# Kernel tuning notes

Hardware: AMD Instinct MI355X
Metric: run time of the kernel (lower is better)

The kernel has to match this reference:

```python
import jax, jax.numpy as jnp
import numpy as np

D, E, H, K = 1024, 8, 1024, 2          # d_model, num_experts, hidden_size, top_k
NUM_LAYERS, LB_W, Z_W = 16, 0.01, 0.001
B, S = 2, 2048


def setup_inputs() -> dict:
    key = jax.random.key(0)
    ks = jax.random.split(key, 8)
    s = lambda d: 1.0 / np.sqrt(d)
    return {
        "x": jax.random.normal(ks[0], (B, S, D), jnp.float32),
        "w_router": jax.random.normal(ks[1], (D, E), jnp.float32) * s(D),
        "w1": jax.random.normal(ks[2], (E, D, H), jnp.float32) * s(D),
        "w3": jax.random.normal(ks[3], (E, D, H), jnp.float32) * s(D),
        "w2": jax.random.normal(ks[4], (E, H, D), jnp.float32) * s(H),
        "sw1": jax.random.normal(ks[5], (D, H), jnp.float32) * s(D),
        "sw3": jax.random.normal(ks[6], (D, H), jnp.float32) * s(D),
        "sw2": jax.random.normal(ks[7], (H, D), jnp.float32) * s(H),
    }


def reference(x, w_router, w1, w3, w2, sw1, sw3, sw2):
    b, s_len, _ = x.shape
    xt = x.reshape(-1, D)                       # (N, D) flattened tokens
    n_tok = xt.shape[0]

    # ---- router: softmax over experts, then top-k ----
    logits = xt @ w_router                      # (N, E)
    probs = jax.nn.softmax(logits, axis=-1)
    weights, indices = jax.lax.top_k(probs, K)  # (N, K)

    # combine weights scattered back to dense (N, E) form
    onehot = jax.nn.one_hot(indices, E, dtype=x.dtype)    # (N, K, E)
    cw = jnp.einsum("nk,nke->ne", weights, onehot)       # (N, E)
    counts = jnp.sum(onehot, axis=(0, 1))                 # (E,) tokens per expert

    # ---- expert SwiGLU MLPs (dense dispatch, weighted combine) ----
    g = jnp.einsum("nd,edh->neh", xt, w1)                 # (N, E, H)
    u = jnp.einsum("nd,edh->neh", xt, w3)
    h = jax.nn.silu(g) * u
    eout = jnp.einsum("neh,ehd->ned", h, w2)              # (N, E, D)
    out = jnp.einsum("ne,ned->nd", cw, eout)              # (N, D)

    # ---- shared expert, weighted-sum combine with top_k ----
    shared = (jax.nn.silu(xt @ sw1) * (xt @ sw3)) @ sw2   # (N, D)
    out = (out * K + shared) / (K + 1)

    # ---- aux losses (training mode) ----
    logits32 = logits.astype(jnp.float32)
    scale = E * LB_W / (NUM_LAYERS * n_tok * K)
    lb_loss = scale * jnp.dot(counts.astype(jnp.float32),
                              jax.nn.softmax(logits32, axis=-1).sum(axis=0))
    z_loss = jnp.mean(jnp.square(jax.nn.logsumexp(logits32, axis=-1))) * Z_W

    return out.reshape(b, s_len, D), lb_loss, z_loss
```

## Files before the change

### kernel.cpp

```cpp
#include <hip/hip_runtime.h>

#define NTOK 4096
#define NEXP 8
#define MAXTILES 104

typedef __attribute__((ext_vector_type(8))) short short8;
typedef __attribute__((ext_vector_type(4))) float f32x4;
typedef __attribute__((ext_vector_type(4))) unsigned int uint4v;
typedef __attribute__((ext_vector_type(2))) unsigned int uint2v;

__device__ __forceinline__ unsigned short f2bf(float f) {
  union { float f; unsigned u; } v; v.f = f;
  unsigned u = v.u;
  return (unsigned short)((u + 0x7FFFu + ((u >> 16) & 1u)) >> 16);
}

__device__ __forceinline__ void gll16(const void* g, void* l) {
  __builtin_amdgcn_global_load_lds((const __attribute__((address_space(1))) void*)g,
                                   (__attribute__((address_space(3))) void*)l, 16, 0, 0);
}

__global__ __launch_bounds__(256) void cvt_t_all_k(
    const float* __restrict__ w1, const float* __restrict__ w3, const float* __restrict__ w2,
    const float* __restrict__ sw1, const float* __restrict__ sw3, const float* __restrict__ sw2,
    unsigned short* __restrict__ dst ) {
  __shared__ unsigned short tile[64][65];
  int z = blockIdx.z;
  const float* S;
  if (z < 8) S = w1 + (size_t)z * 1048576;
  else if (z < 16) S = w3 + (size_t)(z - 8) * 1048576;
  else if (z < 24) S = w2 + (size_t)(z - 16) * 1048576;
  else S = (z == 24) ? sw1 : (z == 25) ? sw3 : sw2;
  unsigned short* Dp = dst + (size_t)z * 1048576;
  int r0 = blockIdx.y * 64, c0 = blockIdx.x * 64;
  int t = threadIdx.x;
  int r = t >> 2, cb = (t & 3) * 16;
  const float* sp = S + (size_t)(r0 + r) * 1024 + c0 + cb;
  f32x4 v0 = ((const f32x4*)sp)[0], v1 = ((const f32x4*)sp)[1];
  f32x4 v2 = ((const f32x4*)sp)[2], v3 = ((const f32x4*)sp)[3];
#pragma unroll
  for (int j = 0; j < 4; ++j) {
    tile[r][cb + j] = f2bf(v0[j]);
    tile[r][cb + 4 + j] = f2bf(v1[j]);
    tile[r][cb + 8 + j] = f2bf(v2[j]);
    tile[r][cb + 12 + j] = f2bf(v3[j]);
  }
  __syncthreads();
  unsigned short* dp = Dp + (size_t)(c0 + r) * 1024 + r0 + cb;
  uint4v o0, o1;
#pragma unroll
  for (int j = 0; j < 4; ++j) {
    o0[j] = (unsigned)tile[cb + 2 * j][r] | ((unsigned)tile[cb + 2 * j + 1][r] << 16);
    o1[j] = (unsigned)tile[cb + 8 + 2 * j][r] | ((unsigned)tile[cb + 9 + 2 * j][r] << 16);
  }
  ((uint4v*)dp)[0] = o0;
  ((uint4v*)dp)[1] = o1;
}

__global__ __launch_bounds__(256) void router_k(
    const float* __restrict__ x, const float* __restrict__ wr, unsigned short* __restrict__ xb,
    int* __restrict__ rec, float* __restrict__ wts, float* __restrict__ probs,
    float* __restrict__ lsebuf) {
  int t = threadIdx.x, lane = t & 63, wv = t >> 6;
  int tok = blockIdx.x * 4 + wv;
  const f32x4* x4 = (const f32x4*)(x + (size_t)tok * 1024);
  f32x4 xv[4];
#pragma unroll
  for (int j = 0; j < 4; ++j) xv[j] = x4[j * 64 + lane];

  unsigned short* xo = xb + (size_t)tok * 1024;
#pragma unroll
  for (int j = 0; j < 4; ++j) {
    uint2v o;
    o[0] = (unsigned)f2bf(xv[j][0]) | ((unsigned)f2bf(xv[j][1]) << 16);
    o[1] = (unsigned)f2bf(xv[j][2]) | ((unsigned)f2bf(xv[j][3]) << 16);
    *(uint2v*)(xo + j * 256 + lane * 4) = o;
  }

  float acc[NEXP];
#pragma unroll
  for (int e = 0; e < NEXP; ++e) acc[e] = 0.f;
#pragma unroll
  for (int j = 0; j < 4; ++j) {
    int base = j * 256 + lane * 4;
#pragma unroll
    for (int c = 0; c < 4; ++c) {
      float xf = xv[j][c];
      const f32x4* wp = (const f32x4*)(wr + (size_t)(base + c) * NEXP);
      f32x4 w0 = wp[0], w1 = wp[1];
#pragma unroll
      for (int e = 0; e < 4; ++e) { acc[e] += xf * w0[e]; acc[4 + e] += xf * w1[e]; }
    }
  }
#pragma unroll
  for (int off = 32; off > 0; off >>= 1) {
#pragma unroll
    for (int e = 0; e < NEXP; ++e) acc[e] += __shfl_xor(acc[e], off);
  }

  float mx = acc[0];
#pragma unroll
  for (int e = 1; e < NEXP; ++e) mx = fmaxf(mx, acc[e]);
  float s = 0.f;
#pragma unroll
  for (int e = 0; e < NEXP; ++e) s += __expf(acc[e] - mx);
  float inv = 1.f / s;

  if (lane < NEXP) probs[(size_t)tok * NEXP + lane] = __expf(acc[lane] - mx) * inv;
  if (lane == 0) {
    int i0 = 0; float v0 = acc[0];
#pragma unroll
    for (int e = 1; e < NEXP; ++e) if (acc[e] > v0) { v0 = acc[e]; i0 = e; }
    int i1 = -1; float v1 = -3.4e38f;
#pragma unroll
    for (int e = 0; e < NEXP; ++e) if (e != i0 && acc[e] > v1) { v1 = acc[e]; i1 = e; }
    rec[tok] = i0 | (i1 << 8);
    wts[2 * tok] = __expf(v0 - mx) * inv;
    wts[2 * tok + 1] = __expf(v1 - mx) * inv;
    lsebuf[tok] = mx + __logf(s);
  }
}

__global__ __launch_bounds__(256) void build_k(
    const int* __restrict__ rec, const float* __restrict__ wts, const float* __restrict__ probs,
    const float* __restrict__ lsebuf,
    int* __restrict__ tlist, float* __restrict__ wlist,
    int* __restrict__ counts, float* __restrict__ probsum, float* __restrict__ zsum) {
  __shared__ int lcnt[NEXP];
  __shared__ int gbase[NEXP];
  __shared__ float wProb[4][NEXP];
  __shared__ float wZ[4];
  int t = threadIdx.x, lane = t & 63, wv = t >> 6;
  if (t < NEXP) lcnt[t] = 0;
  __syncthreads();

  int tok = blockIdx.x * 256 + t;
  int r = rec[tok];
  int i0 = r & 255, i1 = (r >> 8) & 255;
  float w0 = wts[2 * tok], w1 = wts[2 * tok + 1];
  int p0 = atomicAdd(&lcnt[i0], 1);
  int p1 = atomicAdd(&lcnt[i1], 1);

  f32x4 pr0 = ((const f32x4*)(probs + (size_t)tok * NEXP))[0];
  f32x4 pr1 = ((const f32x4*)(probs + (size_t)tok * NEXP))[1];
  float lv = lsebuf[tok];
  float z = lv * lv;
#pragma unroll
  for (int off = 32; off > 0; off >>= 1) {
#pragma unroll
    for (int c = 0; c < 4; ++c) {
      pr0[c] += __shfl_xor(pr0[c], off);
      pr1[c] += __shfl_xor(pr1[c], off);
    }
    z += __shfl_xor(z, off);
  }
  if (lane == 0) {
#pragma unroll
    for (int c = 0; c < 4; ++c) { wProb[wv][c] = pr0[c]; wProb[wv][4 + c] = pr1[c]; }
    wZ[wv] = z;
  }
  __syncthreads();

  if (t < NEXP) {
    gbase[t] = atomicAdd(&counts[t], lcnt[t]);
    atomicAdd(&probsum[t], wProb[0][t] + wProb[1][t] + wProb[2][t] + wProb[3][t]);
  }
  if (t == 0) atomicAdd(zsum, wZ[0] + wZ[1] + wZ[2] + wZ[3]);
  __syncthreads();

  int q0 = gbase[i0] + p0, q1 = gbase[i1] + p1;
  tlist[i0 * NTOK + q0] = tok;
  wlist[i0 * NTOK + q0] = w0;
  tlist[i1 * NTOK + q1] = tok | (1 << 16);
  wlist[i1 * NTOK + q1] = w1;
}

__global__ void scan_k(const int* __restrict__ counts, int* __restrict__ ebase, int* __restrict__ tiles) {
  if (threadIdx.x == 0 && blockIdx.x == 0) {
    int a = 0, t = 0;
    for (int e = 0; e < NEXP; ++e) {
      ebase[e] = a;
      int nt = (counts[e] + 127) >> 7;
      for (int i = 0; i < nt; ++i) tiles[t++] = (e << 16) | i;
      a += nt * 128;
    }
    ebase[NEXP] = a;
    for (int i = 0; i < 32; ++i) tiles[t++] = (NEXP << 16) | i;
    ebase[NEXP + 1] = a + NTOK;
    while (t < MAXTILES) tiles[t++] = -1;
  }
}

__global__ __launch_bounds__(256, 2) void gemm1_k(
    const unsigned short* __restrict__ xb,
    const unsigned short* __restrict__ w1T, const unsigned short* __restrict__ w3T,
    const unsigned short* __restrict__ sw1T, const unsigned short* __restrict__ sw3T,
    unsigned short* __restrict__ hout,
    const int* __restrict__ tlist, const int* __restrict__ counts,
    const int* __restrict__ ebase, const int* __restrict__ tiles) {
  int td = tiles[blockIdx.y];
  if (td < 0) return;
  const int e = td >> 16;
  const int m0 = (td & 0xFFFF) << 7;
  const int n0 = blockIdx.x * 64;
  const bool sh = (e == NEXP);
  const int n_e = sh ? NTOK : counts[e];
  const int hb = ebase[e];
  const unsigned short* B1p = sh ? sw1T : w1T + (size_t)e * 1048576;
  const unsigned short* B3p = sh ? sw3T : w3T + (size_t)e * 1048576;
  const int* listp = tlist + e * NTOK;

  __shared__ unsigned short As[4096], Bs1[2048], Bs3[2048];
  const int tid = threadIdx.x, lane = tid & 63, wv = tid >> 6;
  const int wrw = wv >> 1, wc = wv & 1, l16 = lane & 15, lq = lane >> 4;

  const unsigned short* ga0;
  const unsigned short* ga1;
  const unsigned short* gb;
  const unsigned short* gc;
  {
    int c = tid, r = c >> 2, ks = (c & 3) ^ ((r >> 1) & 3);
    int ar = m0 + r;
    int rowA = sh ? ar : (ar < n_e ? (listp[ar] & 0xFFFF) : 0);
    ga0 = xb + (size_t)rowA * 1024 + ks * 8;
  }
  {
    int c = tid + 256, r = c >> 2, ks = (c & 3) ^ ((r >> 1) & 3);
    int ar = m0 + r;
    int rowA = sh ? ar : (ar < n_e ? (listp[ar] & 0xFFFF) : 0);
    ga1 = xb + (size_t)rowA * 1024 + ks * 8;
  }
  {
    int c = tid, r = c >> 2, ks = (c & 3) ^ ((r >> 1) & 3);
    gb = B1p + (size_t)(n0 + r) * 1024 + ks * 8;
    gc = B3p + (size_t)(n0 + r) * 1024 + ks * 8;
  }
  unsigned short* lA0 = As + wv * 512;
  unsigned short* lA1 = As + 2048 + wv * 512;
  unsigned short* lB = Bs1 + wv * 512;
  unsigned short* lC = Bs3 + wv * 512;

  f32x4 accg[4][2], accu[4][2];
#pragma unroll
  for (int mi = 0; mi < 4; ++mi)
#pragma unroll
    for (int ni = 0; ni < 2; ++ni)
#pragma unroll
      for (int r = 0; r < 4; ++r) { accg[mi][ni][r] = 0.f; accu[mi][ni][r] = 0.f; }

  for (int k0 = 0; k0 < 1024; k0 += 32) {
    gll16(ga0, lA0); gll16(ga1, lA1); gll16(gb, lB); gll16(gc, lC);
    ga0 += 32; ga1 += 32; gb += 32; gc += 32;
    __syncthreads();
    short8 af[4], b1f[2], b3f[2];
#pragma unroll
    for (int mi = 0; mi < 4; ++mi) {
      int R = wrw * 64 + mi * 16 + l16;
      int s = lq ^ ((R >> 1) & 3);
      af[mi] = *(const short8*)&As[R * 32 + s * 8];
    }
#pragma unroll
    for (int ni = 0; ni < 2; ++ni) {
      int R = wc * 32 + ni * 16 + l16;
      int s = lq ^ ((R >> 1) & 3);
      b1f[ni] = *(const short8*)&Bs1[R * 32 + s * 8];
      b3f[ni] = *(const short8*)&Bs3[R * 32 + s * 8];
    }
#pragma unroll
    for (int mi = 0; mi < 4; ++mi)
#pragma unroll
      for (int ni = 0; ni < 2; ++ni) {
        accg[mi][ni] = __builtin_amdgcn_mfma_f32_16x16x32_bf16(af[mi], b1f[ni], accg[mi][ni], 0, 0, 0);
        accu[mi][ni] = __builtin_amdgcn_mfma_f32_16x16x32_bf16(af[mi], b3f[ni], accu[mi][ni], 0, 0, 0);
      }
    __syncthreads();
  }

#pragma unroll
  for (int mi = 0; mi < 4; ++mi)
#pragma unroll
    for (int ni = 0; ni < 2; ++ni) {
      int col = n0 + wc * 32 + ni * 16 + l16;
#pragma unroll
      for (int r = 0; r < 4; ++r) {
        int row = m0 + wrw * 64 + mi * 16 + lq * 4 + r;
        float g = accg[mi][ni][r], u = accu[mi][ni][r];
        float h = g / (1.f + __expf(-g)) * u;
        hout[(size_t)(hb + row) * 1024 + col] = (row < n_e) ? f2bf(h) : (unsigned short)0;
      }
    }
}

__global__ __launch_bounds__(256, 2) void gemm2_k(
    const unsigned short* __restrict__ hbuf,
    const unsigned short* __restrict__ w2T, const unsigned short* __restrict__ sw2T,
    float* __restrict__ yout,
    const int* __restrict__ tlist, const float* __restrict__ wlist,
    const int* __restrict__ counts, const int* __restrict__ ebase, const int* __restrict__ tiles) {
  int td = tiles[blockIdx.y];
  if (td < 0) return;
  const int e = td >> 16;
  const int m0 = (td & 0xFFFF) << 7;
  const int n0 = blockIdx.x * 128;
  const bool sh = (e == NEXP);
  const int n_e = sh ? NTOK : counts[e];
  const int hb = ebase[e];
  const unsigned short* Bp = sh ? sw2T : w2T + (size_t)e * 1048576;
  const int* listp = tlist + e * NTOK;

  __shared__ unsigned short As[4096], Bs[4096];
  const int tid = threadIdx.x, lane = tid & 63, wv = tid >> 6;
  const int wrw = wv >> 1, wc = wv & 1, l16 = lane & 15, lq = lane >> 4;

  const unsigned short* ga[2];
  const unsigned short* gb[2];
#pragma unroll
  for (int i = 0; i < 2; ++i) {
    int c = tid + i * 256;
    int r = c >> 2, kc = c & 3;
    int ks = kc ^ ((r >> 1) & 3);
    ga[i] = hbuf + (size_t)(hb + m0 + r) * 1024 + ks * 8;
    gb[i] = Bp + (size_t)(n0 + r) * 1024 + ks * 8;
  }
  unsigned short* lA[2] = {As + wv * 512, As + 2048 + wv * 512};
  unsigned short* lB[2] = {Bs + wv * 512, Bs + 2048 + wv * 512};

  f32x4 acc[4][4];
#pragma unroll
  for (int mi = 0; mi < 4; ++mi)
#pragma unroll
    for (int ni = 0; ni < 4; ++ni)
#pragma unroll
      for (int r = 0; r < 4; ++r) acc[mi][ni][r] = 0.f;

  for (int k0 = 0; k0 < 1024; k0 += 32) {
#pragma unroll
    for (int i = 0; i < 2; ++i) {
      gll16(ga[i], lA[i]); gll16(gb[i], lB[i]);
      ga[i] += 32; gb[i] += 32;
    }
    __syncthreads();
    short8 af[4], bf[4];
#pragma unroll
    for (int mi = 0; mi < 4; ++mi) {
      int R = wrw * 64 + mi * 16 + l16;
      int s = lq ^ ((R >> 1) & 3);
      af[mi] = *(const short8*)&As[R * 32 + s * 8];
    }
#pragma unroll
    for (int ni = 0; ni < 4; ++ni) {
      int R = wc * 64 + ni * 16 + l16;
      int s = lq ^ ((R >> 1) & 3);
      bf[ni] = *(const short8*)&Bs[R * 32 + s * 8];
    }
#pragma unroll
    for (int mi = 0; mi < 4; ++mi)
#pragma unroll
      for (int ni = 0; ni < 4; ++ni)
        acc[mi][ni] = __builtin_amdgcn_mfma_f32_16x16x32_bf16(af[mi], bf[ni], acc[mi][ni], 0, 0, 0);
    __syncthreads();
  }

#pragma unroll
  for (int mi = 0; mi < 4; ++mi)
#pragma unroll
    for (int r = 0; r < 4; ++r) {
      int row = m0 + wrw * 64 + mi * 16 + lq * 4 + r;
      if (sh) {
        float* yp = yout + ((size_t)2 * NTOK + row) * 1024 + n0 + wc * 64 + l16;
#pragma unroll
        for (int ni = 0; ni < 4; ++ni) yp[ni * 16] = acc[mi][ni][r] * (1.f / 3.f);
      } else if (row < n_e) {
        int ent = listp[row];
        float wt = wlist[e * NTOK + row] * (2.f / 3.f);
        int tok = ent & 0xFFFF, ks = ent >> 16;
        float* yp = yout + ((size_t)ks * NTOK + tok) * 1024 + n0 + wc * 64 + l16;
#pragma unroll
        for (int ni = 0; ni < 4; ++ni) yp[ni * 16] = wt * acc[mi][ni][r];
      }
    }
}

__global__ __launch_bounds__(256) void combine_k(const float* __restrict__ y,
                                                 float* __restrict__ out) {
  size_t i = (size_t)blockIdx.x * 256 + threadIdx.x;
  const f32x4* y0 = (const f32x4*)y + i;
  const f32x4* y1 = y0 + (NTOK * 1024 / 4);
  const f32x4* y2 = y1 + (NTOK * 1024 / 4);
  ((f32x4*)out)[i] = *y0 + *y1 + *y2;
}

__global__ void losses_k(const int* __restrict__ counts, const float* __restrict__ probsum,
                         const float* __restrict__ zsum, float* __restrict__ out) {
  if (threadIdx.x == 0 && blockIdx.x == 0) {
    float dot = 0.f;
    for (int e = 0; e < NEXP; ++e) dot += (float)counts[e] * probsum[e];
    out[0] = 6.103515625e-7f * dot;
    out[1] = zsum[0] * (0.001f / 4096.f);
  }
}

extern "C" void kernel_launch(void* const* d_in, const int* in_sizes, int n_in,
                              void* d_out, int out_size, void* d_ws, size_t ws_size,
                              hipStream_t stream) {
  const float* x   = (const float*)d_in[0];
  const float* wrt = (const float*)d_in[1];
  const float* w1  = (const float*)d_in[2];
  const float* w3  = (const float*)d_in[3];
  const float* w2  = (const float*)d_in[4];
  const float* sw1 = (const float*)d_in[5];
  const float* sw3 = (const float*)d_in[6];
  const float* sw2 = (const float*)d_in[7];
  float* out = (float*)d_out;

  char* p = (char*)d_ws;
  auto alloc = [&](size_t b) { char* r = p; p += (b + 255) & ~(size_t)255; return r; };
  unsigned short* xb   = (unsigned short*)alloc((size_t)NTOK * 1024 * 2);
  unsigned short* w1T  = (unsigned short*)alloc((size_t)27 * 1048576 * 2);
  unsigned short* w3T  = w1T + (size_t)8 * 1048576;
  unsigned short* w2T  = w3T + (size_t)8 * 1048576;
  unsigned short* sw1T = w2T + (size_t)8 * 1048576;
  unsigned short* sw3T = sw1T + 1048576;
  unsigned short* sw2T = sw3T + 1048576;
  unsigned short* hbuf = (unsigned short*)alloc((size_t)13312 * 1024 * 2);
  float* ybuf   = (float*)alloc((size_t)3 * NTOK * 1024 * 4);
  int* tlist    = (int*)alloc((size_t)NEXP * NTOK * 4);
  float* wlist  = (float*)alloc((size_t)NEXP * NTOK * 4);
  int* rec      = (int*)alloc((size_t)NTOK * 4);
  float* wts    = (float*)alloc((size_t)NTOK * 2 * 4);
  float* probs  = (float*)alloc((size_t)NTOK * NEXP * 4);
  float* lsebuf = (float*)alloc((size_t)NTOK * 4);
  int* tiles    = (int*)alloc(MAXTILES * 4);
  int* ebase    = (int*)alloc(256);
  char* stats   = alloc(768);
  int* counts   = (int*)stats;
  float* probsum = (float*)(stats + 256);
  float* zsum    = (float*)(stats + 512);

  (void)hipMemsetAsync(stats, 0, 768, stream);

  cvt_t_all_k<<<dim3(16, 16, 27), 256, 0, stream>>>(w1, w3, w2, sw1, sw3, sw2, w1T);
  router_k<<<1024, 256, 0, stream>>>(x, wrt, xb, rec, wts, probs, lsebuf);
  build_k<<<16, 256, 0, stream>>>(rec, wts, probs, lsebuf, tlist, wlist, counts, probsum, zsum);
  scan_k<<<1, 64, 0, stream>>>(counts, ebase, tiles);
  gemm1_k<<<dim3(16, MAXTILES), 256, 0, stream>>>(xb, w1T, w3T, sw1T, sw3T, hbuf, tlist, counts, ebase, tiles);
  gemm2_k<<<dim3(8, MAXTILES), 256, 0, stream>>>(hbuf, w2T, sw2T, ybuf, tlist, wlist, counts, ebase, tiles);
  combine_k<<<NTOK * 1024 / 4 / 256, 256, 0, stream>>>(ybuf, out);
  losses_k<<<1, 64, 0, stream>>>(counts, probsum, zsum, out + (size_t)NTOK * 1024);
}
```

Baseline: 320.4 us.

## Fuse combine into gemm2 via atomic adds and deepen K tile to 64

gemm2 now accumulates routed and shared-expert outputs directly into the output with float atomicAdd, which removes the 48MB staging buffer and the separate combine kernel. The output is zeroed with a memset first. Both GEMMs also move from a K-step of 32 to 64 with a new 8-way XOR swizzle, which halves the number of barrier iterations. The launch-bounds occupancy hint rises from 2 to 3. In exchange, atomics add contention and make the summation order nondeterministic, and the larger LDS footprint (32KB per block in both GEMMs) may limit occupancy.

```diff
diff --git a/kernel.cpp b/kernel.cpp
--- a/kernel.cpp
+++ b/kernel.cpp
@@ -171,7 +171,7 @@
   int q0 = gbase[i0] + p0, q1 = gbase[i1] + p1;
   tlist[i0 * NTOK + q0] = tok;
   wlist[i0 * NTOK + q0] = w0;
-  tlist[i1 * NTOK + q1] = tok | (1 << 16);
+  tlist[i1 * NTOK + q1] = tok;
   wlist[i1 * NTOK + q1] = w1;
 }
 
@@ -191,7 +191,7 @@
   }
 }
 
-__global__ __launch_bounds__(256, 2) void gemm1_k(
+__global__ __launch_bounds__(256, 3) void gemm1_k(
     const unsigned short* __restrict__ xb,
     const unsigned short* __restrict__ w1T, const unsigned short* __restrict__ w3T,
     const unsigned short* __restrict__ sw1T, const unsigned short* __restrict__ sw3T,
@@ -210,35 +210,33 @@
   const unsigned short* B3p = sh ? sw3T : w3T + (size_t)e * 1048576;
   const int* listp = tlist + e * NTOK;
 
-  __shared__ unsigned short As[4096], Bs1[2048], Bs3[2048];
+  __shared__ unsigned short As[128 * 64], Bs1[64 * 64], Bs3[64 * 64];
   const int tid = threadIdx.x, lane = tid & 63, wv = tid >> 6;
   const int wrw = wv >> 1, wc = wv & 1, l16 = lane & 15, lq = lane >> 4;
 
-  const unsigned short* ga0;
-  const unsigned short* ga1;
-  const unsigned short* gb;
-  const unsigned short* gc;
-  {
-    int c = tid, r = c >> 2, ks = (c & 3) ^ ((r >> 1) & 3);
+  const unsigned short* ga[4];
+#pragma unroll
+  for (int i = 0; i < 4; ++i) {
+    int c = tid + i * 256;
+    int r = c >> 3, ks = (c & 7) ^ (r & 7);
     int ar = m0 + r;
     int rowA = sh ? ar : (ar < n_e ? (listp[ar] & 0xFFFF) : 0);
-    ga0 = xb + (size_t)rowA * 1024 + ks * 8;
-  }
-  {
-    int c = tid + 256, r = c >> 2, ks = (c & 3) ^ ((r >> 1) & 3);
-    int ar = m0 + r;
-    int rowA = sh ? ar : (ar < n_e ? (listp[ar] & 0xFFFF) : 0);
-    ga1 = xb + (size_t)rowA * 1024 + ks * 8;
-  }
-  {
-    int c = tid, r = c >> 2, ks = (c & 3) ^ ((r >> 1) & 3);
-    gb = B1p + (size_t)(n0 + r) * 1024 + ks * 8;
-    gc = B3p + (size_t)(n0 + r) * 1024 + ks * 8;
-  }
-  unsigned short* lA0 = As + wv * 512;
-  unsigned short* lA1 = As + 2048 + wv * 512;
-  unsigned short* lB = Bs1 + wv * 512;
-  unsigned short* lC = Bs3 + wv * 512;
+    ga[i] = xb + (size_t)rowA * 1024 + ks * 8;
+  }
+  const unsigned short* gb[2];
+  const unsigned short* gc[2];
+#pragma unroll
+  for (int i = 0; i < 2; ++i) {
+    int c = tid + i * 256;
+    int r = c >> 3, ks = (c & 7) ^ (r & 7);
+    gb[i] = B1p + (size_t)(n0 + r) * 1024 + ks * 8;
+    gc[i] = B3p + (size_t)(n0 + r) * 1024 + ks * 8;
+  }
+  unsigned short* lA[4];
+#pragma unroll
+  for (int i = 0; i < 4; ++i) lA[i] = As + i * 2048 + wv * 512;
+  unsigned short* lB[2] = {Bs1 + wv * 512, Bs1 + 2048 + wv * 512};
+  unsigned short* lC[2] = {Bs3 + wv * 512, Bs3 + 2048 + wv * 512};
 
   f32x4 accg[4][2], accu[4][2];
 #pragma unroll
@@ -248,31 +246,36 @@
 #pragma unroll
       for (int r = 0; r < 4; ++r) { accg[mi][ni][r] = 0.f; accu[mi][ni][r] = 0.f; }
 
-  for (int k0 = 0; k0 < 1024; k0 += 32) {
-    gll16(ga0, lA0); gll16(ga1, lA1); gll16(gb, lB); gll16(gc, lC);
-    ga0 += 32; ga1 += 32; gb += 32; gc += 32;
+  for (int k0 = 0; k0 < 1024; k0 += 64) {
+#pragma unroll
+    for (int i = 0; i < 4; ++i) { gll16(ga[i], lA[i]); ga[i] += 64; }
+#pragma unroll
+    for (int i = 0; i < 2; ++i) { gll16(gb[i], lB[i]); gb[i] += 64; gll16(gc[i], lC[i]); gc[i] += 64; }
     __syncthreads();
-    short8 af[4], b1f[2], b3f[2];
-#pragma unroll
-    for (int mi = 0; mi < 4; ++mi) {
-      int R = wrw * 64 + mi * 16 + l16;
-      int s = lq ^ ((R >> 1) & 3);
-      af[mi] = *(const short8*)&As[R * 32 + s * 8];
-    }
-#pragma unroll
-    for (int ni = 0; ni < 2; ++ni) {
-      int R = wc * 32 + ni * 16 + l16;
-      int s = lq ^ ((R >> 1) & 3);
-      b1f[ni] = *(const short8*)&Bs1[R * 32 + s * 8];
-      b3f[ni] = *(const short8*)&Bs3[R * 32 + s * 8];
-    }
-#pragma unroll
-    for (int mi = 0; mi < 4; ++mi)
+#pragma unroll
+    for (int kh = 0; kh < 2; ++kh) {
+      short8 af[4], b1f[2], b3f[2];
+#pragma unroll
+      for (int mi = 0; mi < 4; ++mi) {
+        int R = wrw * 64 + mi * 16 + l16;
+        int s = (kh * 4 + lq) ^ (R & 7);
+        af[mi] = *(const short8*)&As[R * 64 + s * 8];
+      }
 #pragma unroll
       for (int ni = 0; ni < 2; ++ni) {
-        accg[mi][ni] = __builtin_amdgcn_mfma_f32_16x16x32_bf16(af[mi], b1f[ni], accg[mi][ni], 0, 0, 0);
-        accu[mi][ni] = __builtin_amdgcn_mfma_f32_16x16x32_bf16(af[mi], b3f[ni], accu[mi][ni], 0, 0, 0);
-      }
+        int R = wc * 32 + ni * 16 + l16;
+        int s = (kh * 4 + lq) ^ (R & 7);
+        b1f[ni] = *(const short8*)&Bs1[R * 64 + s * 8];
+        b3f[ni] = *(const short8*)&Bs3[R * 64 + s * 8];
+      }
+#pragma unroll
+      for (int mi = 0; mi < 4; ++mi)
+#pragma unroll
+        for (int ni = 0; ni < 2; ++ni) {
+          accg[mi][ni] = __builtin_amdgcn_mfma_f32_16x16x32_bf16(af[mi], b1f[ni], accg[mi][ni], 0, 0, 0);
+          accu[mi][ni] = __builtin_amdgcn_mfma_f32_16x16x32_bf16(af[mi], b3f[ni], accu[mi][ni], 0, 0, 0);
+        }
+    }
     __syncthreads();
   }
 
@@ -291,10 +294,10 @@
     }
 }
 
-__global__ __launch_bounds__(256, 2) void gemm2_k(
+__global__ __launch_bounds__(256, 3) void gemm2_k(
     const unsigned short* __restrict__ hbuf,
     const unsigned short* __restrict__ w2T, const unsigned short* __restrict__ sw2T,
-    float* __restrict__ yout,
+    float* __restrict__ out,
     const int* __restrict__ tlist, const float* __restrict__ wlist,
     const int* __restrict__ counts, const int* __restrict__ ebase, const int* __restrict__ tiles) {
   int td = tiles[blockIdx.y];
@@ -308,22 +311,26 @@
   const unsigned short* Bp = sh ? sw2T : w2T + (size_t)e * 1048576;
   const int* listp = tlist + e * NTOK;
 
-  __shared__ unsigned short As[4096], Bs[4096];
+  __shared__ unsigned short As[128 * 64], Bs[128 * 64];
   const int tid = threadIdx.x, lane = tid & 63, wv = tid >> 6;
   const int wrw = wv >> 1, wc = wv & 1, l16 = lane & 15, lq = lane >> 4;
 
-  const unsigned short* ga[2];
-  const unsigned short* gb[2];
-#pragma unroll
-  for (int i = 0; i < 2; ++i) {
+  const unsigned short* ga[4];
+  const unsigned short* gb[4];
+#pragma unroll
+  for (int i = 0; i < 4; ++i) {
     int c = tid + i * 256;
-    int r = c >> 2, kc = c & 3;
-    int ks = kc ^ ((r >> 1) & 3);
+    int r = c >> 3, ks = (c & 7) ^ (r & 7);
     ga[i] = hbuf + (size_t)(hb + m0 + r) * 1024 + ks * 8;
     gb[i] = Bp + (size_t)(n0 + r) * 1024 + ks * 8;
   }
-  unsigned short* lA[2] = {As + wv * 512, As + 2048 + wv * 512};
-  unsigned short* lB[2] = {Bs + wv * 512, Bs + 2048 + wv * 512};
+  unsigned short* lA[4];
+  unsigned short* lB[4];
+#pragma unroll
+  for (int i = 0; i < 4; ++i) {
+    lA[i] = As + i * 2048 + wv * 512;
+    lB[i] = Bs + i * 2048 + wv * 512;
+  }
 
   f32x4 acc[4][4];
 #pragma unroll
@@ -333,31 +340,34 @@
 #pragma unroll
       for (int r = 0; r < 4; ++r) acc[mi][ni][r] = 0.f;
 
-  for (int k0 = 0; k0 < 1024; k0 += 32) {
-#pragma unroll
-    for (int i = 0; i < 2; ++i) {
-      gll16(ga[i], lA[i]); gll16(gb[i], lB[i]);
-      ga[i] += 32; gb[i] += 32;
+  for (int k0 = 0; k0 < 1024; k0 += 64) {
+#pragma unroll
+    for (int i = 0; i < 4; ++i) {
+      gll16(ga[i], lA[i]); ga[i] += 64;
+      gll16(gb[i], lB[i]); gb[i] += 64;
     }
     __syncthreads();
-    short8 af[4], bf[4];
-#pragma unroll
-    for (int mi = 0; mi < 4; ++mi) {
-      int R = wrw * 64 + mi * 16 + l16;
-      int s = lq ^ ((R >> 1) & 3);
-      af[mi] = *(const short8*)&As[R * 32 + s * 8];
-    }
-#pragma unroll
-    for (int ni = 0; ni < 4; ++ni) {
-      int R = wc * 64 + ni * 16 + l16;
-      int s = lq ^ ((R >> 1) & 3);
-      bf[ni] = *(const short8*)&Bs[R * 32 + s * 8];
-    }
-#pragma unroll
-    for (int mi = 0; mi < 4; ++mi)
-#pragma unroll
-      for (int ni = 0; ni < 4; ++ni)
-        acc[mi][ni] = __builtin_amdgcn_mfma_f32_16x16x32_bf16(af[mi], bf[ni], acc[mi][ni], 0, 0, 0);
+#pragma unroll
+    for (int kh = 0; kh < 2; ++kh) {
+      short8 af[4], bf[4];
+#pragma unroll
+      for (int mi = 0; mi < 4; ++mi) {
+        int R = wrw * 64 + mi * 16 + l16;
+        int s = (kh * 4 + lq) ^ (R & 7);
+        af[mi] = *(const short8*)&As[R * 64 + s * 8];
+      }
+#pragma unroll
+      for (int ni = 0; ni < 4; ++ni) {
+        int R = wc * 64 + ni * 16 + l16;
+        int s = (kh * 4 + lq) ^ (R & 7);
+        bf[ni] = *(const short8*)&Bs[R * 64 + s * 8];
+      }
+#pragma unroll
+      for (int mi = 0; mi < 4; ++mi)
+#pragma unroll
+        for (int ni = 0; ni < 4; ++ni)
+          acc[mi][ni] = __builtin_amdgcn_mfma_f32_16x16x32_bf16(af[mi], bf[ni], acc[mi][ni], 0, 0, 0);
+    }
     __syncthreads();
   }
 
@@ -367,27 +377,17 @@
     for (int r = 0; r < 4; ++r) {
       int row = m0 + wrw * 64 + mi * 16 + lq * 4 + r;
       if (sh) {
-        float* yp = yout + ((size_t)2 * NTOK + row) * 1024 + n0 + wc * 64 + l16;
-#pragma unroll
-        for (int ni = 0; ni < 4; ++ni) yp[ni * 16] = acc[mi][ni][r] * (1.f / 3.f);
+        float* yp = out + (size_t)row * 1024 + n0 + wc * 64 + l16;
+#pragma unroll
+        for (int ni = 0; ni < 4; ++ni) atomicAdd(&yp[ni * 16], acc[mi][ni][r] * (1.f / 3.f));
       } else if (row < n_e) {
-        int ent = listp[row];
+        int tok = listp[row] & 0xFFFF;
         float wt = wlist[e * NTOK + row] * (2.f / 3.f);
-        int tok = ent & 0xFFFF, ks = ent >> 16;
-        float* yp = yout + ((size_t)ks * NTOK + tok) * 1024 + n0 + wc * 64 + l16;
-#pragma unroll
-        for (int ni = 0; ni < 4; ++ni) yp[ni * 16] = wt * acc[mi][ni][r];
-      }
-    }
-}
-
-__global__ __launch_bounds__(256) void combine_k(const float* __restrict__ y,
-                                                 float* __restrict__ out) {
-  size_t i = (size_t)blockIdx.x * 256 + threadIdx.x;
-  const f32x4* y0 = (const f32x4*)y + i;
-  const f32x4* y1 = y0 + (NTOK * 1024 / 4);
-  const f32x4* y2 = y1 + (NTOK * 1024 / 4);
-  ((f32x4*)out)[i] = *y0 + *y1 + *y2;
+        float* yp = out + (size_t)tok * 1024 + n0 + wc * 64 + l16;
+#pragma unroll
+        for (int ni = 0; ni < 4; ++ni) atomicAdd(&yp[ni * 16], wt * acc[mi][ni][r]);
+      }
+    }
 }
 
 __global__ void losses_k(const int* __restrict__ counts, const float* __restrict__ probsum,
@@ -423,7 +423,6 @@
   unsigned short* sw3T = sw1T + 1048576;
   unsigned short* sw2T = sw3T + 1048576;
   unsigned short* hbuf = (unsigned short*)alloc((size_t)13312 * 1024 * 2);
-  float* ybuf   = (float*)alloc((size_t)3 * NTOK * 1024 * 4);
   int* tlist    = (int*)alloc((size_t)NEXP * NTOK * 4);
   float* wlist  = (float*)alloc((size_t)NEXP * NTOK * 4);
   int* rec      = (int*)alloc((size_t)NTOK * 4);
@@ -438,13 +437,13 @@
   float* zsum    = (float*)(stats + 512);
 
   (void)hipMemsetAsync(stats, 0, 768, stream);
+  (void)hipMemsetAsync(out, 0, (size_t)out_size * 4, stream);
 
   cvt_t_all_k<<<dim3(16, 16, 27), 256, 0, stream>>>(w1, w3, w2, sw1, sw3, sw2, w1T);
   router_k<<<1024, 256, 0, stream>>>(x, wrt, xb, rec, wts, probs, lsebuf);
   build_k<<<16, 256, 0, stream>>>(rec, wts, probs, lsebuf, tlist, wlist, counts, probsum, zsum);
   scan_k<<<1, 64, 0, stream>>>(counts, ebase, tiles);
   gemm1_k<<<dim3(16, MAXTILES), 256, 0, stream>>>(xb, w1T, w3T, sw1T, sw3T, hbuf, tlist, counts, ebase, tiles);
-  gemm2_k<<<dim3(8, MAXTILES), 256, 0, stream>>>(hbuf, w2T, sw2T, ybuf, tlist, wlist, counts, ebase, tiles);
-  combine_k<<<NTOK * 1024 / 4 / 256, 256, 0, stream>>>(ybuf, out);
+  gemm2_k<<<dim3(8, MAXTILES), 256, 0, stream>>>(hbuf, w2T, sw2T, out, tlist, wlist, counts, ebase, tiles);
   losses_k<<<1, 64, 0, stream>>>(counts, probsum, zsum, out + (size_t)NTOK * 1024);
 }
```

Measured after the change: 326.7 us. About the same (+2.0%).
